# Optimization experiments

Measured on AMD Instinct MI355X. Metric: run time of the kernel, lower is better.

## Reference

```python
import jax, jax.numpy as jnp
import numpy as np

N = 50000
E = 800000
D_IN, D_HID, D_OUT = 128, 128, 64


def setup_inputs() -> dict:
    key = jax.random.key(0)
    ks = jax.random.split(key, 8)
    x = jax.random.normal(ks[0], (N, D_IN), dtype=jnp.float32)
    edge_index = jax.random.randint(ks[1], (2, E), 0, N, dtype=jnp.int64)
    # Glorot-ish init for weights
    W1 = jax.random.normal(ks[2], (D_IN, D_HID), dtype=jnp.float32) / np.sqrt(D_IN)
    b1 = jnp.zeros((D_HID,), dtype=jnp.float32)
    W2 = jax.random.normal(ks[3], (D_HID, D_OUT), dtype=jnp.float32) / np.sqrt(D_HID)
    b2 = jnp.zeros((D_OUT,), dtype=jnp.float32)
    fc_W = jax.random.normal(ks[4], (D_OUT, D_OUT), dtype=jnp.float32) / np.sqrt(D_OUT)
    fc_b = jnp.zeros((D_OUT,), dtype=jnp.float32)
    return {"x": x, "edge_index": edge_index, "W1": W1, "b1": b1,
            "W2": W2, "b2": b2, "fc_W": fc_W, "fc_b": fc_b}


def _gcn_norm(edge_index, n_nodes):
    # PyG GCNConv default: add self-loops, symmetric normalization
    src, dst = edge_index[0], edge_index[1]
    loops = jnp.arange(n_nodes, dtype=edge_index.dtype)
    src = jnp.concatenate([src, loops])
    dst = jnp.concatenate([dst, loops])
    deg = jax.ops.segment_sum(jnp.ones_like(dst, dtype=jnp.float32), dst,
                              num_segments=n_nodes)
    dinv = jnp.where(deg > 0, jax.lax.rsqrt(deg), 0.0)
    norm = dinv[src] * dinv[dst]  # [E + N]
    return src, dst, norm


def _gcn_conv(x, src, dst, norm, W, b):
    h = x @ W                          # [N, d_out] transform first (fewer FLOPs)
    msg = h[src] * norm[:, None]       # gather + scale  [E+N, d_out]
    out = jax.ops.segment_sum(msg, dst, num_segments=x.shape[0])
    return out + b


def reference(x, edge_index, W1, b1, W2, b2, fc_W, fc_b):
    src, dst, norm = _gcn_norm(edge_index, x.shape[0])
    h = jax.nn.relu(_gcn_conv(x, src, dst, norm, W1, b1))
    h = jax.nn.relu(_gcn_conv(h, src, dst, norm, W2, b2))
    return h @ fc_W + fc_b
```

## Files before the change

kernel.cpp:

```cpp
#include <hip/hip_runtime.h>
#include <hip/hip_bf16.h>


typedef __attribute__((ext_vector_type(8))) short bf16x8;
typedef __attribute__((ext_vector_type(4))) float f32x4;

#define SLAB 64
#define BCAP 6144
#define BINCH 8192

__device__ __forceinline__ unsigned short f2bf(float f) {
    unsigned u = __float_as_uint(f);
    unsigned r = (u + 0x7FFFu + ((u >> 16) & 1u)) >> 16;
    return (unsigned short)r;
}
__device__ __forceinline__ float bf16_lo(unsigned u) {
    return __uint_as_float((u & 0xFFFFu) << 16);
}
__device__ __forceinline__ float bf16_hi(unsigned u) {
    return __uint_as_float(u & 0xFFFF0000u);
}

#define UNPK16(cA, cB, ci)                                        \
    ci[0] = cA.x & 0xFFFFu;  ci[1] = cA.x >> 16;                  \
    ci[2] = cA.y & 0xFFFFu;  ci[3] = cA.y >> 16;                  \
    ci[4] = cA.z & 0xFFFFu;  ci[5] = cA.z >> 16;                  \
    ci[6] = cA.w & 0xFFFFu;  ci[7] = cA.w >> 16;                  \
    ci[8] = cB.x & 0xFFFFu;  ci[9] = cB.x >> 16;                  \
    ci[10] = cB.y & 0xFFFFu; ci[11] = cB.y >> 16;                 \
    ci[12] = cB.z & 0xFFFFu; ci[13] = cB.z >> 16;                 \
    ci[14] = cB.w & 0xFFFFu; ci[15] = cB.w >> 16;


__global__ void k_wt(const float* __restrict__ W1, const float* __restrict__ W2,
                     const float* __restrict__ fcW,
                     unsigned short* __restrict__ W1T, unsigned short* __restrict__ W2T,
                     unsigned short* __restrict__ fcWT, int* __restrict__ gcnt,
                     unsigned short* __restrict__ hs1r, unsigned short* __restrict__ hs2,
                     int n) {
    int j = blockIdx.x * blockDim.x + threadIdx.x;
    if (j < 256) gcnt[j] = 0;
    if (j < 16384) {
        int m = j >> 7, k = j & 127;
        W1T[j] = f2bf(W1[k * 128 + m]);
    } else if (j < 24576) {
        int q = j - 16384;
        int m = q >> 7, k = q & 127;
        W2T[q] = f2bf(W2[k * 64 + m]);
    } else if (j < 28672) {
        int q = j - 24576;
        int m = q >> 6, k = q & 63;
        fcWT[q] = f2bf(fcW[k * 64 + m]);
    } else if (j < 28800) {
        hs1r[(size_t)n * 128 + (j - 28672)] = 0;
    } else if (j < 28864) {
        hs2[(size_t)n * 64 + (j - 28800)] = 0;
    }
}


__device__ __forceinline__ void gemm1_body(const float* __restrict__ X,
                                           const unsigned short* __restrict__ W1T,
                                           unsigned short* __restrict__ outp,
                                           int n, int blk, int tid,
                                           unsigned short* xs) {
    constexpr int LDW = 136;
    int base = blk * 64;
    for (int idx = tid; idx < 64 * 32; idx += 256) {
        int r = idx >> 5, c = idx & 31;
        int row = base + r;
        float4 v = make_float4(0.f, 0.f, 0.f, 0.f);
        if (row < n) v = ((const float4*)X)[(size_t)row * 32 + c];
        unsigned short* dp = &xs[r * LDW + c * 4];
        dp[0] = f2bf(v.x); dp[1] = f2bf(v.y); dp[2] = f2bf(v.z); dp[3] = f2bf(v.w);
    }
    __syncthreads();

    int wave = tid >> 6, lane = tid & 63;
    int quad = lane >> 4, l16 = lane & 15;
    int rbase = wave * 16;

    bf16x8 af[4];
#pragma unroll
    for (int kb = 0; kb < 4; ++kb)
        af[kb] = *(const bf16x8*)&xs[(rbase + l16) * LDW + kb * 32 + quad * 8];

#pragma unroll
    for (int jt = 0; jt < 8; ++jt) {
        f32x4 acc = {0.f, 0.f, 0.f, 0.f};
#pragma unroll
        for (int kb = 0; kb < 4; ++kb) {
            bf16x8 bf = *(const bf16x8*)&W1T[(size_t)(jt * 16 + l16) * 128 + kb * 32 + quad * 8];
            acc = __builtin_amdgcn_mfma_f32_16x16x32_bf16(af[kb], bf, acc, 0, 0, 0);
        }
#pragma unroll
        for (int r = 0; r < 4; ++r) {
            int row = base + rbase + quad * 4 + r;
            if (row < n)
                outp[(size_t)row * 128 + jt * 16 + l16] = f2bf(acc[r]);
        }
    }
}


__global__ __launch_bounds__(1024) void k_front(
    const int* __restrict__ src, const int* __restrict__ dst, int e,
    int* __restrict__ gcnt, unsigned* __restrict__ staging,
    const float* __restrict__ x, const unsigned short* __restrict__ W1T,
    unsigned short* __restrict__ hs1r, int n, int nbk, int ngemm) {
    __shared__ __align__(16) unsigned short xs4[4][64 * 136];
    __shared__ int bcnt[256], bpos[256], gofs[256];
    int bid = (int)blockIdx.x, tid = (int)threadIdx.x;

    if (bid < ngemm) {
        int tile = tid >> 8;
        gemm1_body(x, W1T, hs1r, n, bid * 4 + tile, tid & 255, xs4[tile]);
    } else {
        int b0 = bid - ngemm;
        if (tid < 256) { bcnt[tid] = 0; bpos[tid] = 0; }
        __syncthreads();
        int e0 = b0 * BINCH;
        int d[8], s[8];
#pragma unroll
        for (int r = 0; r < 8; ++r) {
            int i = e0 + r * 1024 + tid;
            if (i < e) { d[r] = dst[i]; s[r] = src[i]; } else d[r] = -1;
        }
#pragma unroll
        for (int r = 0; r < 8; ++r)
            if (d[r] >= 0) atomicAdd(&bcnt[d[r] >> 8], 1);
        __syncthreads();
        if (tid < nbk) {
            int c = bcnt[tid];
            gofs[tid] = c ? atomicAdd(&gcnt[tid], c) : 0;
        }
        __syncthreads();
#pragma unroll
        for (int r = 0; r < 8; ++r) {
            if (d[r] >= 0) {
                int b = d[r] >> 8;
                int p = atomicAdd(&bpos[b], 1);
                int idx = gofs[b] + p;
                if (idx < BCAP)
                    staging[(size_t)b * BCAP + idx] =
                        ((unsigned)d[r] << 16) | (unsigned)s[r];
            }
        }
    }
}


__global__ __launch_bounds__(1024) void k_scatter(
    const unsigned* __restrict__ staging, const int* __restrict__ gcnt,
    int* __restrict__ cnt, unsigned short* __restrict__ col,
    float* __restrict__ dinv, unsigned* __restrict__ hs1u, int n) {
    __shared__ int lcnt[256];
    __shared__ __align__(16) unsigned short ls[256 * SLAB];
    __shared__ float sdi[256];
    int b = (int)blockIdx.x, t = (int)threadIdx.x;
    if (t < 256) lcnt[t] = 0;
    unsigned sent2 = (unsigned)n | ((unsigned)n << 16);
    for (int i = t; i < 256 * SLAB / 2; i += 1024) ((unsigned*)ls)[i] = sent2;
    __syncthreads();
    int eb = gcnt[b]; if (eb > BCAP) eb = BCAP;
    const unsigned* sp = staging + (size_t)b * BCAP;
    for (int i = t; i < eb; i += 1024) {
        unsigned pk = sp[i];
        int dl = (int)(pk >> 16) & 255;
        int pos = atomicAdd(&lcnt[dl], 1);
        if (pos < SLAB) ls[(dl << 6) + pos] = (unsigned short)(pk & 0xFFFFu);
    }
    __syncthreads();
    int base = b << 8;
    const uint4* lsv = (const uint4*)ls;
    uint4* gv = (uint4*)(col + ((size_t)base << 6));
    for (int i = t; i < 256 * SLAB / 8; i += 1024) gv[i] = lsv[i];
    if (t < 256) {
        int c = lcnt[t];
        float dv = rsqrtf((float)c + 1.0f);
        sdi[t] = dv;
        cnt[base + t] = c;
        dinv[base + t] = dv;
    }
    __syncthreads();
    int rows = n - base; if (rows > 256) rows = 256; if (rows < 0) rows = 0;
    unsigned* hp = hs1u + ((size_t)base << 6);
    for (int i = t; i < rows * 64; i += 1024) {
        int r = i >> 6;
        unsigned u = hp[i];
        float sc = sdi[r];
        unsigned lo = f2bf(sc * bf16_lo(u));
        unsigned hi = f2bf(sc * bf16_hi(u));
        hp[i] = lo | (hi << 16);
    }
}


__global__ __launch_bounds__(256) void k_aggg128(
    const int* __restrict__ cnt, const unsigned short* __restrict__ col,
    const unsigned short* __restrict__ hs, const float* __restrict__ dinv,
    const float* __restrict__ bias, const unsigned short* __restrict__ W2T,
    unsigned short* __restrict__ hs2, int n) {
    __shared__ __align__(16) unsigned short ys[16 * 136];
    __shared__ float ldi[16];
    int tid = (int)threadIdx.x;
    int w = tid >> 6, lane = tid & 63;
    int half = lane >> 5, l32 = lane & 31;
    int gbase = (int)blockIdx.x * 16;
    const uint2* hp2 = (const uint2*)hs;

    int n0 = gbase + w * 4 + half;
    int n1 = n0 + 2;
    int c0 = cnt[n0]; if (c0 > SLAB) c0 = SLAB;
    int c1 = cnt[n1]; if (c1 > SLAB) c1 = SLAB;
    int dm = c0 > c1 ? c0 : c1;
    int dmo = __shfl_xor(dm, 32);
    if (dmo > dm) dm = dmo;

    const unsigned short* cp0 = &col[(size_t)n0 * SLAB];
    const unsigned short* cp1 = &col[(size_t)n1 * SLAB];
    float di0 = dinv[n0], di1 = dinv[n1];
    int h0 = n0 < n ? n0 : n, h1 = n1 < n ? n1 : n;
    uint2 s0 = hp2[(size_t)h0 * 32 + l32];
    uint2 s1 = hp2[(size_t)h1 * 32 + l32];
    float a0 = bf16_lo(s0.x), a1 = bf16_hi(s0.x), a2 = bf16_lo(s0.y), a3 = bf16_hi(s0.y);
    float b0 = bf16_lo(s1.x), b1 = bf16_hi(s1.x), b2 = bf16_lo(s1.y), b3 = bf16_hi(s1.y);

    for (int i = 0; i < dm; i += 16) {
        uint4 cA0 = *(const uint4*)&cp0[i];
        uint4 cB0 = *(const uint4*)&cp0[i + 8];
        uint4 cA1 = *(const uint4*)&cp1[i];
        uint4 cB1 = *(const uint4*)&cp1[i + 8];
        unsigned ci0[16], ci1[16];
        UNPK16(cA0, cB0, ci0)
        UNPK16(cA1, cB1, ci1)
        uint2 u0[16], u1[16];
#pragma unroll
        for (int j = 0; j < 16; ++j) u0[j] = hp2[(size_t)ci0[j] * 32 + l32];
#pragma unroll
        for (int j = 0; j < 16; ++j) u1[j] = hp2[(size_t)ci1[j] * 32 + l32];
#pragma unroll
        for (int j = 0; j < 16; ++j) {
            a0 += bf16_lo(u0[j].x); a1 += bf16_hi(u0[j].x);
            a2 += bf16_lo(u0[j].y); a3 += bf16_hi(u0[j].y);
            b0 += bf16_lo(u1[j].x); b1 += bf16_hi(u1[j].x);
            b2 += bf16_lo(u1[j].y); b3 += bf16_hi(u1[j].y);
        }
    }

    float4 bv = *(const float4*)&bias[l32 * 4];
    {
        float v0 = fmaxf(di0 * a0 + bv.x, 0.0f);
        float v1 = fmaxf(di0 * a1 + bv.y, 0.0f);
        float v2 = fmaxf(di0 * a2 + bv.z, 0.0f);
        float v3 = fmaxf(di0 * a3 + bv.w, 0.0f);
        unsigned o0 = (unsigned)f2bf(v0) | ((unsigned)f2bf(v1) << 16);
        unsigned o1 = (unsigned)f2bf(v2) | ((unsigned)f2bf(v3) << 16);
        *(uint2*)((char*)ys + (size_t)(w * 4 + half) * 272 + l32 * 8) = make_uint2(o0, o1);
    }
    {
        float v0 = fmaxf(di1 * b0 + bv.x, 0.0f);
        float v1 = fmaxf(di1 * b1 + bv.y, 0.0f);
        float v2 = fmaxf(di1 * b2 + bv.z, 0.0f);
        float v3 = fmaxf(di1 * b3 + bv.w, 0.0f);
        unsigned o0 = (unsigned)f2bf(v0) | ((unsigned)f2bf(v1) << 16);
        unsigned o1 = (unsigned)f2bf(v2) | ((unsigned)f2bf(v3) << 16);
        *(uint2*)((char*)ys + (size_t)(w * 4 + 2 + half) * 272 + l32 * 8) = make_uint2(o0, o1);
    }
    if (l32 == 0) { ldi[w * 4 + half] = di0; ldi[w * 4 + 2 + half] = di1; }
    __syncthreads();

    int quad = lane >> 4, l16 = lane & 15;
    bf16x8 a[4];
#pragma unroll
    for (int kb = 0; kb < 4; ++kb)
        a[kb] = *(const bf16x8*)&ys[l16 * 136 + kb * 32 + quad * 8];
    f32x4 acc = {0.f, 0.f, 0.f, 0.f};
#pragma unroll
    for (int kb = 0; kb < 4; ++kb) {
        bf16x8 bf = *(const bf16x8*)&W2T[(size_t)(w * 16 + l16) * 128 + kb * 32 + quad * 8];
        acc = __builtin_amdgcn_mfma_f32_16x16x32_bf16(a[kb], bf, acc, 0, 0, 0);
    }
#pragma unroll
    for (int r = 0; r < 4; ++r) {
        int lrow = quad * 4 + r;
        int row = gbase + lrow;
        if (row < n)
            hs2[(size_t)row * 64 + w * 16 + l16] = f2bf(acc[r] * ldi[lrow]);
    }
}


__global__ __launch_bounds__(256) void k_aggg64(
    const int* __restrict__ cnt, const unsigned short* __restrict__ col,
    const unsigned short* __restrict__ hs, const float* __restrict__ dinv,
    const float* __restrict__ bias, const unsigned short* __restrict__ fcWT,
    const float* __restrict__ fcb, float* __restrict__ out, int n) {
    __shared__ __align__(16) unsigned short yt[16 * 72];
    int tid = (int)threadIdx.x;
    int w = tid >> 6, lane = tid & 63;
    int half = lane >> 5, l32 = lane & 31;
    int gbase = (int)blockIdx.x * 16;
    const unsigned* hp = (const unsigned*)hs;

    int n0 = gbase + w * 4 + half;
    int n1 = n0 + 2;
    int c0 = cnt[n0]; if (c0 > SLAB) c0 = SLAB;
    int c1 = cnt[n1]; if (c1 > SLAB) c1 = SLAB;
    int dm = c0 > c1 ? c0 : c1;
    int dmo = __shfl_xor(dm, 32);
    if (dmo > dm) dm = dmo;

    const unsigned short* cp0 = &col[(size_t)n0 * SLAB];
    const unsigned short* cp1 = &col[(size_t)n1 * SLAB];
    float di0 = dinv[n0], di1 = dinv[n1];
    int h0 = n0 < n ? n0 : n, h1 = n1 < n ? n1 : n;
    unsigned s0 = hp[(size_t)h0 * 32 + l32];
    unsigned s1 = hp[(size_t)h1 * 32 + l32];
    float a0 = bf16_lo(s0), a1 = bf16_hi(s0);
    float b0 = bf16_lo(s1), b1 = bf16_hi(s1);

    for (int i = 0; i < dm; i += 16) {
        uint4 cA0 = *(const uint4*)&cp0[i];
        uint4 cB0 = *(const uint4*)&cp0[i + 8];
        uint4 cA1 = *(const uint4*)&cp1[i];
        uint4 cB1 = *(const uint4*)&cp1[i + 8];
        unsigned ci0[16], ci1[16];
        UNPK16(cA0, cB0, ci0)
        UNPK16(cA1, cB1, ci1)
        unsigned u0[16], u1[16];
#pragma unroll
        for (int j = 0; j < 16; ++j) u0[j] = hp[(size_t)ci0[j] * 32 + l32];
#pragma unroll
        for (int j = 0; j < 16; ++j) u1[j] = hp[(size_t)ci1[j] * 32 + l32];
#pragma unroll
        for (int j = 0; j < 16; ++j) {
            a0 += bf16_lo(u0[j]); a1 += bf16_hi(u0[j]);
            b0 += bf16_lo(u1[j]); b1 += bf16_hi(u1[j]);
        }
    }

    float2 bv = *(const float2*)&bias[l32 * 2];
    {
        float v0 = fmaxf(di0 * a0 + bv.x, 0.0f);
        float v1 = fmaxf(di0 * a1 + bv.y, 0.0f);
        *(unsigned*)((char*)yt + (size_t)(w * 4 + half) * 144 + l32 * 4) =
            (unsigned)f2bf(v0) | ((unsigned)f2bf(v1) << 16);
    }
    {
        float v0 = fmaxf(di1 * b0 + bv.x, 0.0f);
        float v1 = fmaxf(di1 * b1 + bv.y, 0.0f);
        *(unsigned*)((char*)yt + (size_t)(w * 4 + 2 + half) * 144 + l32 * 4) =
            (unsigned)f2bf(v0) | ((unsigned)f2bf(v1) << 16);
    }
    __syncthreads();

    int quad = lane >> 4, l16 = lane & 15;
    bf16x8 a[2];
#pragma unroll
    for (int kb = 0; kb < 2; ++kb)
        a[kb] = *(const bf16x8*)&yt[l16 * 72 + kb * 32 + quad * 8];
    f32x4 acc = {0.f, 0.f, 0.f, 0.f};
#pragma unroll
    for (int kb = 0; kb < 2; ++kb) {
        bf16x8 bf = *(const bf16x8*)&fcWT[(size_t)(w * 16 + l16) * 64 + kb * 32 + quad * 8];
        acc = __builtin_amdgcn_mfma_f32_16x16x32_bf16(a[kb], bf, acc, 0, 0, 0);
    }
    float bv2 = fcb[w * 16 + l16];
#pragma unroll
    for (int r = 0; r < 4; ++r) {
        int row = gbase + quad * 4 + r;
        if (row < n)
            out[(size_t)row * 64 + w * 16 + l16] = acc[r] + bv2;
    }
}


extern "C" void kernel_launch(void* const* d_in, const int* in_sizes, int n_in,
                              void* d_out, int out_size, void* d_ws, size_t ws_size,
                              hipStream_t stream) {
    const float* x   = (const float*)d_in[0];
    const int*   ei  = (const int*)d_in[1];
    const float* W1  = (const float*)d_in[2];
    const float* b1  = (const float*)d_in[3];
    const float* W2  = (const float*)d_in[4];
    const float* b2  = (const float*)d_in[5];
    const float* fcW = (const float*)d_in[6];
    const float* fcb = (const float*)d_in[7];
    float* out = (float*)d_out;

    const int N = in_sizes[0] / 128;
    const int E = in_sizes[1] / 2;
    const int* src = ei;
    const int* dst = ei + E;

    const int NB    = (N + 255) >> 8;
    const int Npad  = NB << 8;
    const int nbin  = (E + BINCH - 1) / BINCH;
    const int gg64  = (N + 63) / 64;
    const int ngemm = (gg64 + 3) / 4;
    const int nagg  = (N + 15) / 16;

    auto align16 = [](size_t v) { return (v + 15) & ~(size_t)15; };
    char* p = (char*)d_ws;
    int* gcnt = (int*)p;                       p += align16(sizeof(int) * 256);
    unsigned* staging = (unsigned*)p;          p += align16(sizeof(unsigned) * (size_t)NB * BCAP);
    int* cnt = (int*)p;                        p += align16(sizeof(int) * Npad);
    float* dinv = (float*)p;                   p += align16(sizeof(float) * Npad);
    unsigned short* col = (unsigned short*)p;  p += align16(sizeof(unsigned short) * (size_t)Npad * SLAB);
    unsigned short* W1T = (unsigned short*)p;  p += align16(2 * 128 * 128);
    unsigned short* W2T = (unsigned short*)p;  p += align16(2 * 64 * 128);
    unsigned short* fcWT = (unsigned short*)p; p += align16(2 * 64 * 64);
    unsigned short* hs1r = (unsigned short*)p; p += align16(2 * ((size_t)N + 1) * 128);
    unsigned short* hs2 = (unsigned short*)p;  p += align16(2 * ((size_t)N + 1) * 64);

    k_wt<<<114, 256, 0, stream>>>(W1, W2, fcW, W1T, W2T, fcWT, gcnt,
                                  hs1r, hs2, N);

    k_front<<<ngemm + nbin, 1024, 0, stream>>>(src, dst, E, gcnt, staging,
                                               x, W1T, hs1r, N, NB, ngemm);
    k_scatter<<<NB, 1024, 0, stream>>>(staging, gcnt, cnt, col, dinv,
                                       (unsigned*)hs1r, N);

    k_aggg128<<<nagg, 256, 0, stream>>>(cnt, col, hs1r, dinv, b1, W2T, hs2, N);

    k_aggg64<<<nagg, 256, 0, stream>>>(cnt, col, hs2, dinv, b2, fcWT, fcb, out, N);
}
```

Baseline: 176.2 us.

## Drop weight-prep kernel and global atomics by per-bin private staging segments

Removes the separate weight-transpose launch: GEMM blocks now load and transpose W1 into swizzled LDS themselves, and one binning block converts W2/fcW and zeroes the pad rows. Edge binning switches from global atomic offsets into a shared per-bucket buffer to fixed 60 chunks, each writing private per-bucket segments with counts. The scatter kernel then walks all chunk segments per bucket. This removes a launch and the global atomics, but each GEMM block redoes the W1 conversion, blocks shrink to 512 threads, and per-segment capacity caps could drop edges under skewed inputs.

```diff
diff --git a/kernel.cpp b/kernel.cpp
--- a/kernel.cpp
+++ b/kernel.cpp
@@ -6,8 +6,8 @@
 typedef __attribute__((ext_vector_type(4))) float f32x4;
 
 #define SLAB 64
-#define BCAP 6144
-#define BINCH 8192
+#define SCAP 160
+#define NBIN 60
 
 __device__ __forceinline__ unsigned short f2bf(float f) {
     unsigned u = __float_as_uint(f);
@@ -32,143 +32,132 @@
     ci[14] = cB.w & 0xFFFFu; ci[15] = cB.w >> 16;
 
 
-__global__ void k_wt(const float* __restrict__ W1, const float* __restrict__ W2,
-                     const float* __restrict__ fcW,
-                     unsigned short* __restrict__ W1T, unsigned short* __restrict__ W2T,
-                     unsigned short* __restrict__ fcWT, int* __restrict__ gcnt,
-                     unsigned short* __restrict__ hs1r, unsigned short* __restrict__ hs2,
-                     int n) {
-    int j = blockIdx.x * blockDim.x + threadIdx.x;
-    if (j < 256) gcnt[j] = 0;
-    if (j < 16384) {
-        int m = j >> 7, k = j & 127;
-        W1T[j] = f2bf(W1[k * 128 + m]);
-    } else if (j < 24576) {
-        int q = j - 16384;
-        int m = q >> 7, k = q & 127;
-        W2T[q] = f2bf(W2[k * 64 + m]);
-    } else if (j < 28672) {
-        int q = j - 24576;
-        int m = q >> 6, k = q & 63;
-        fcWT[q] = f2bf(fcW[k * 64 + m]);
-    } else if (j < 28800) {
-        hs1r[(size_t)n * 128 + (j - 28672)] = 0;
-    } else if (j < 28864) {
-        hs2[(size_t)n * 64 + (j - 28800)] = 0;
-    }
-}
-
-
-__device__ __forceinline__ void gemm1_body(const float* __restrict__ X,
-                                           const unsigned short* __restrict__ W1T,
-                                           unsigned short* __restrict__ outp,
-                                           int n, int blk, int tid,
-                                           unsigned short* xs) {
-    constexpr int LDW = 136;
-    int base = blk * 64;
-    for (int idx = tid; idx < 64 * 32; idx += 256) {
-        int r = idx >> 5, c = idx & 31;
-        int row = base + r;
-        float4 v = make_float4(0.f, 0.f, 0.f, 0.f);
-        if (row < n) v = ((const float4*)X)[(size_t)row * 32 + c];
-        unsigned short* dp = &xs[r * LDW + c * 4];
-        dp[0] = f2bf(v.x); dp[1] = f2bf(v.y); dp[2] = f2bf(v.z); dp[3] = f2bf(v.w);
-    }
-    __syncthreads();
-
-    int wave = tid >> 6, lane = tid & 63;
-    int quad = lane >> 4, l16 = lane & 15;
-    int rbase = wave * 16;
-
-    bf16x8 af[4];
-#pragma unroll
-    for (int kb = 0; kb < 4; ++kb)
-        af[kb] = *(const bf16x8*)&xs[(rbase + l16) * LDW + kb * 32 + quad * 8];
-
-#pragma unroll
-    for (int jt = 0; jt < 8; ++jt) {
-        f32x4 acc = {0.f, 0.f, 0.f, 0.f};
-#pragma unroll
-        for (int kb = 0; kb < 4; ++kb) {
-            bf16x8 bf = *(const bf16x8*)&W1T[(size_t)(jt * 16 + l16) * 128 + kb * 32 + quad * 8];
-            acc = __builtin_amdgcn_mfma_f32_16x16x32_bf16(af[kb], bf, acc, 0, 0, 0);
-        }
-#pragma unroll
-        for (int r = 0; r < 4; ++r) {
-            int row = base + rbase + quad * 4 + r;
-            if (row < n)
-                outp[(size_t)row * 128 + jt * 16 + l16] = f2bf(acc[r]);
-        }
-    }
-}
-
-
-__global__ __launch_bounds__(1024) void k_front(
+__global__ __launch_bounds__(512) void k_front(
     const int* __restrict__ src, const int* __restrict__ dst, int e,
-    int* __restrict__ gcnt, unsigned* __restrict__ staging,
-    const float* __restrict__ x, const unsigned short* __restrict__ W1T,
-    unsigned short* __restrict__ hs1r, int n, int nbk, int ngemm) {
-    __shared__ __align__(16) unsigned short xs4[4][64 * 136];
-    __shared__ int bcnt[256], bpos[256], gofs[256];
+    unsigned* __restrict__ staging, int* __restrict__ bincnt,
+    const float* __restrict__ x, const float* __restrict__ W1,
+    const float* __restrict__ W2, const float* __restrict__ fcW,
+    unsigned short* __restrict__ W2T, unsigned short* __restrict__ fcWT,
+    unsigned short* __restrict__ hs1r, unsigned short* __restrict__ hs2,
+    int n, int nb, int ngemm, int nbin, int binch) {
+    __shared__ __align__(16) unsigned short xs2[2][64 * 136];
+    __shared__ __align__(16) unsigned short wlds[128 * 128];
+    __shared__ int bcnt[256], bpos[256];
     int bid = (int)blockIdx.x, tid = (int)threadIdx.x;
 
     if (bid < ngemm) {
-        int tile = tid >> 8;
-        gemm1_body(x, W1T, hs1r, n, bid * 4 + tile, tid & 255, xs4[tile]);
+        for (int j = tid; j < 16384; j += 512) {
+            int k = j >> 7, m = j & 127;
+            wlds[m * 128 + (k ^ ((m & 7) << 3))] = f2bf(W1[j]);
+        }
+        __syncthreads();
+
+        constexpr int LDW = 136;
+        int tile = tid >> 8, t = tid & 255;
+        unsigned short* xs = xs2[tile];
+        int blk = bid * 2 + tile;
+        int base = blk * 64;
+        for (int idx = t; idx < 64 * 32; idx += 256) {
+            int r = idx >> 5, c = idx & 31;
+            int row = base + r;
+            float4 v = make_float4(0.f, 0.f, 0.f, 0.f);
+            if (row < n) v = ((const float4*)x)[(size_t)row * 32 + c];
+            unsigned short* dp = &xs[r * LDW + c * 4];
+            dp[0] = f2bf(v.x); dp[1] = f2bf(v.y); dp[2] = f2bf(v.z); dp[3] = f2bf(v.w);
+        }
+        __syncthreads();
+
+        int wave = t >> 6, lane = t & 63;
+        int quad = lane >> 4, l16 = lane & 15;
+        int rbase = wave * 16;
+
+        bf16x8 af[4];
+#pragma unroll
+        for (int kb = 0; kb < 4; ++kb)
+            af[kb] = *(const bf16x8*)&xs[(rbase + l16) * LDW + kb * 32 + quad * 8];
+
+#pragma unroll
+        for (int jt = 0; jt < 8; ++jt) {
+            f32x4 acc = {0.f, 0.f, 0.f, 0.f};
+            int m = jt * 16 + l16;
+            int sw = (l16 & 7) << 3;
+#pragma unroll
+            for (int kb = 0; kb < 4; ++kb) {
+                bf16x8 bf = *(const bf16x8*)&wlds[m * 128 + ((kb * 32 + quad * 8) ^ sw)];
+                acc = __builtin_amdgcn_mfma_f32_16x16x32_bf16(af[kb], bf, acc, 0, 0, 0);
+            }
+#pragma unroll
+            for (int r = 0; r < 4; ++r) {
+                int row = base + rbase + quad * 4 + r;
+                if (row < n)
+                    hs1r[(size_t)row * 128 + jt * 16 + l16] = f2bf(acc[r]);
+            }
+        }
     } else {
-        int b0 = bid - ngemm;
-        if (tid < 256) { bcnt[tid] = 0; bpos[tid] = 0; }
+        int c = bid - ngemm;
+        if (c == 0) {
+            for (int j = tid; j < 12480; j += 512) {
+                if (j < 8192) {
+                    int m = j >> 7, k = j & 127;
+                    W2T[j] = f2bf(W2[k * 64 + m]);
+                } else if (j < 12288) {
+                    int q = j - 8192;
+                    int m = q >> 6, k = q & 63;
+                    fcWT[q] = f2bf(fcW[k * 64 + m]);
+                } else if (j < 12416) {
+                    hs1r[(size_t)n * 128 + (j - 12288)] = 0;
+                } else {
+                    hs2[(size_t)n * 64 + (j - 12416)] = 0;
+                }
+            }
+        }
+        for (int i = tid; i < 256; i += 512) { bcnt[i] = 0; bpos[i] = 0; }
         __syncthreads();
-        int e0 = b0 * BINCH;
-        int d[8], s[8];
-#pragma unroll
-        for (int r = 0; r < 8; ++r) {
-            int i = e0 + r * 1024 + tid;
-            if (i < e) { d[r] = dst[i]; s[r] = src[i]; } else d[r] = -1;
-        }
-#pragma unroll
-        for (int r = 0; r < 8; ++r)
-            if (d[r] >= 0) atomicAdd(&bcnt[d[r] >> 8], 1);
+        int e0 = c * binch;
+        int lim = e - e0; if (lim > binch) lim = binch; if (lim < 0) lim = 0;
+        for (int i = tid; i < lim; i += 512)
+            atomicAdd(&bcnt[dst[e0 + i] >> 8], 1);
         __syncthreads();
-        if (tid < nbk) {
-            int c = bcnt[tid];
-            gofs[tid] = c ? atomicAdd(&gcnt[tid], c) : 0;
+        for (int i = tid; i < nb; i += 512) {
+            int v = bcnt[i];
+            bincnt[c * nb + i] = v < SCAP ? v : SCAP;
         }
         __syncthreads();
-#pragma unroll
-        for (int r = 0; r < 8; ++r) {
-            if (d[r] >= 0) {
-                int b = d[r] >> 8;
-                int p = atomicAdd(&bpos[b], 1);
-                int idx = gofs[b] + p;
-                if (idx < BCAP)
-                    staging[(size_t)b * BCAP + idx] =
-                        ((unsigned)d[r] << 16) | (unsigned)s[r];
-            }
+        for (int i = tid; i < lim; i += 512) {
+            int d = dst[e0 + i], s = src[e0 + i];
+            int b = d >> 8;
+            int p = atomicAdd(&bpos[b], 1);
+            if (p < SCAP)
+                staging[((size_t)c * nb + b) * SCAP + p] = ((unsigned)d << 16) | (unsigned)s;
         }
     }
 }
 
 
 __global__ __launch_bounds__(1024) void k_scatter(
-    const unsigned* __restrict__ staging, const int* __restrict__ gcnt,
+    const unsigned* __restrict__ staging, const int* __restrict__ bincnt,
     int* __restrict__ cnt, unsigned short* __restrict__ col,
-    float* __restrict__ dinv, unsigned* __restrict__ hs1u, int n) {
+    float* __restrict__ dinv, unsigned* __restrict__ hs1u, int n, int nb, int nbin) {
     __shared__ int lcnt[256];
     __shared__ __align__(16) unsigned short ls[256 * SLAB];
     __shared__ float sdi[256];
+    __shared__ int scnt[64];
     int b = (int)blockIdx.x, t = (int)threadIdx.x;
     if (t < 256) lcnt[t] = 0;
+    if (t < nbin) scnt[t] = bincnt[t * nb + b];
     unsigned sent2 = (unsigned)n | ((unsigned)n << 16);
     for (int i = t; i < 256 * SLAB / 2; i += 1024) ((unsigned*)ls)[i] = sent2;
     __syncthreads();
-    int eb = gcnt[b]; if (eb > BCAP) eb = BCAP;
-    const unsigned* sp = staging + (size_t)b * BCAP;
-    for (int i = t; i < eb; i += 1024) {
-        unsigned pk = sp[i];
-        int dl = (int)(pk >> 16) & 255;
-        int pos = atomicAdd(&lcnt[dl], 1);
-        if (pos < SLAB) ls[(dl << 6) + pos] = (unsigned short)(pk & 0xFFFFu);
+    int g = t >> 6, l = t & 63;
+    for (int c = g; c < nbin; c += 16) {
+        int ccnt = scnt[c];
+        const unsigned* seg = staging + ((size_t)c * nb + b) * SCAP;
+        for (int i = l; i < ccnt; i += 64) {
+            unsigned pk = seg[i];
+            int dl = (int)(pk >> 16) & 255;
+            int pos = atomicAdd(&lcnt[dl], 1);
+            if (pos < SLAB) ls[(dl << 6) + pos] = (unsigned short)(pk & 0xFFFFu);
+        }
     }
     __syncthreads();
     int base = b << 8;
@@ -396,31 +385,30 @@
 
     const int NB    = (N + 255) >> 8;
     const int Npad  = NB << 8;
-    const int nbin  = (E + BINCH - 1) / BINCH;
-    const int gg64  = (N + 63) / 64;
-    const int ngemm = (gg64 + 3) / 4;
+    const int nbin  = NBIN;
+    const int binch = (E + nbin - 1) / nbin;
+    const int ngt   = (N + 63) / 64;
+    const int ngemm = (ngt + 1) / 2;
     const int nagg  = (N + 15) / 16;
 
     auto align16 = [](size_t v) { return (v + 15) & ~(size_t)15; };
     char* p = (char*)d_ws;
-    int* gcnt = (int*)p;                       p += align16(sizeof(int) * 256);
-    unsigned* staging = (unsigned*)p;          p += align16(sizeof(unsigned) * (size_t)NB * BCAP);
+    unsigned* staging = (unsigned*)p;          p += align16(sizeof(unsigned) * (size_t)nbin * NB * SCAP);
+    int* bincnt = (int*)p;                     p += align16(sizeof(int) * (size_t)nbin * NB);
     int* cnt = (int*)p;                        p += align16(sizeof(int) * Npad);
     float* dinv = (float*)p;                   p += align16(sizeof(float) * Npad);
     unsigned short* col = (unsigned short*)p;  p += align16(sizeof(unsigned short) * (size_t)Npad * SLAB);
-    unsigned short* W1T = (unsigned short*)p;  p += align16(2 * 128 * 128);
     unsigned short* W2T = (unsigned short*)p;  p += align16(2 * 64 * 128);
     unsigned short* fcWT = (unsigned short*)p; p += align16(2 * 64 * 64);
     unsigned short* hs1r = (unsigned short*)p; p += align16(2 * ((size_t)N + 1) * 128);
     unsigned short* hs2 = (unsigned short*)p;  p += align16(2 * ((size_t)N + 1) * 64);
 
-    k_wt<<<114, 256, 0, stream>>>(W1, W2, fcW, W1T, W2T, fcWT, gcnt,
-                                  hs1r, hs2, N);
-
-    k_front<<<ngemm + nbin, 1024, 0, stream>>>(src, dst, E, gcnt, staging,
-                                               x, W1T, hs1r, N, NB, ngemm);
-    k_scatter<<<NB, 1024, 0, stream>>>(staging, gcnt, cnt, col, dinv,
-                                       (unsigned*)hs1r, N);
+    k_front<<<ngemm + nbin, 512, 0, stream>>>(src, dst, E, staging, bincnt,
+                                              x, W1, W2, fcW, W2T, fcWT,
+                                              hs1r, hs2, N, NB, ngemm, nbin, binch);
+
+    k_scatter<<<NB, 1024, 0, stream>>>(staging, bincnt, cnt, col, dinv,
+                                       (unsigned*)hs1r, N, NB, nbin);
 
     k_aggg128<<<nagg, 256, 0, stream>>>(cnt, col, hs1r, dinv, b1, W2T, hs2, N);
 
```

New measurement: 187.0 us. +6.1%, slower.
